# Optimization experiments

Hardware: AMD Instinct MI355X
Metric: run time of the kernel (lower is better)

The kernel has to match this reference:

```python
import jax, jax.numpy as jnp
import numpy as np

TEMP = 0.1
QUEUE_SIZE = 512
CUTOFF_KM = 25.0
EARTH_R_KM = 6371.0088


def _normalize(x, eps=1e-12):
    # F.normalize: x / max(||x||, eps)
    n = jnp.linalg.norm(x, axis=-1, keepdims=True)
    return x / jnp.maximum(n, eps)


def _haversine_km(g1, g2):
    # g1: (B,2) [lat,lon] degrees; g2: (S,2) -> (B,S) great-circle km
    r = jnp.pi / 180.0
    lat1 = g1[:, 0:1] * r
    lon1 = g1[:, 1:2] * r
    lat2 = g2[None, :, 0] * r
    lon2 = g2[None, :, 1] * r
    dlat = lat2 - lat1
    dlon = lon2 - lon1
    a = jnp.sin(dlat / 2) ** 2 + jnp.cos(lat1) * jnp.cos(lat2) * jnp.sin(dlon / 2) ** 2
    return 2.0 * EARTH_R_KM * jnp.arcsin(jnp.sqrt(jnp.clip(a, 0.0, 1.0)))


def setup_inputs() -> dict:
    key = jax.random.key(0)
    k = jax.random.split(key, 7)
    n_aug, B, D, S = 4, 256, 768, 65536
    V = jax.random.normal(k[0], (n_aug, B, D), jnp.float32)
    L = jax.random.normal(k[1], (B, D), jnp.float32)
    gps = jnp.concatenate([
        jax.random.uniform(k[2], (B, 1), jnp.float32, -90.0, 90.0),
        jax.random.uniform(k[3], (B, 1), jnp.float32, -180.0, 180.0)], axis=1)
    support_features = jax.random.normal(k[4], (S, D), jnp.float32)
    support_gps = jnp.concatenate([
        jax.random.uniform(k[5], (S, 1), jnp.float32, -90.0, 90.0),
        jax.random.uniform(k[6], (S, 1), jnp.float32, -180.0, 180.0)], axis=1)
    return {"V": V, "L": L, "gps": gps,
            "support_features": support_features, "support_gps": support_gps}


def reference(V, L, gps, support_features, support_gps):
    # org joint embedding always from V[0]; nearest neighbour over raw support feats
    org = _normalize(V[0] * L)                                   # (B,D)
    sim = org @ support_features.T                               # (B,S)
    nn_idx = jnp.argmax(sim, axis=1)                             # (B,)
    nn = _normalize(support_features[nn_idx])                    # (B,D)

    # augmented joints for j = 1..n_aug-1
    augs = _normalize(V[1:] * L[None])                           # (J,B,D)
    # numerator always uses V[1] (as in the original code), constant over j
    num = jnp.einsum('bd,bd->b', nn, augs[0]) / TEMP             # (B,)

    # in-batch denominator: sum_i exp(nn_b . aug_{j,i} / T)
    batch_den = jnp.exp(jnp.einsum('bd,jid->jbi', nn, augs) / TEMP).sum(axis=2)  # (J,B)

    # GPS-filtered negative queue: first QUEUE_SIZE support entries > 25 km away,
    # zero-padded (zero rows contribute exp(0) = 1, matching the torch code)
    mask = _haversine_km(gps, support_gps) > CUTOFF_KM           # (B,S)
    order = jnp.argsort(jnp.where(mask, 0, 1), axis=1)[:, :QUEUE_SIZE]  # stable: kept in original order
    valid = jnp.take_along_axis(mask, order, axis=1)             # (B,Q)
    qfeat = support_features[order] * valid[..., None]           # (B,Q,D)
    queue_den = jnp.exp(jnp.einsum('bd,bqd->bq', nn, qfeat) / TEMP).sum(axis=1)  # (B,)

    den = jnp.log(batch_den + queue_den[None, :])                # (J,B)
    loss = -(num[None, :] - den).sum() / V.shape[1]
    return loss
```

## Files before the change

kernel.cpp:

```cpp
#include <hip/hip_runtime.h>
#include <hip/hip_bf16.h>

#define B_ROWS 256
#define S_SUP  65536
#define D_DIM  768
#define QSZ    512
#define NCH    3
#define CHUNK_K 256
#define ACH_BYTES 131072

typedef short bf16x8 __attribute__((ext_vector_type(8)));
typedef float f32x4  __attribute__((ext_vector_type(4)));
typedef float f32x16 __attribute__((ext_vector_type(16)));

__device__ __forceinline__ bf16x8 cvt8(float4 a, float4 b) {
  bf16x8 r;
  r[0] = (short)(__float_as_uint(a.x) >> 16);
  r[1] = (short)(__float_as_uint(a.y) >> 16);
  r[2] = (short)(__float_as_uint(a.z) >> 16);
  r[3] = (short)(__float_as_uint(a.w) >> 16);
  r[4] = (short)(__float_as_uint(b.x) >> 16);
  r[5] = (short)(__float_as_uint(b.y) >> 16);
  r[6] = (short)(__float_as_uint(b.z) >> 16);
  r[7] = (short)(__float_as_uint(b.w) >> 16);
  return r;
}

__device__ __forceinline__ void gl_lds16(const void* g, void* l) {
  __builtin_amdgcn_global_load_lds(
      (const __attribute__((address_space(1))) unsigned int*)g,
      (__attribute__((address_space(3))) unsigned int*)l, 16, 0, 0);
}

__device__ __forceinline__ float block_sum(float v) {
  __shared__ float tmp[4];
  #pragma unroll
  for (int m = 32; m >= 1; m >>= 1) v += __shfl_xor(v, m, 64);
  __syncthreads();
  if ((threadIdx.x & 63) == 0) tmp[threadIdx.x >> 6] = v;
  __syncthreads();
  return tmp[0] + tmp[1] + tmp[2] + tmp[3];
}

__device__ __forceinline__ double block_sum_d(double v) {
  __shared__ double tmp[4];
  #pragma unroll
  for (int m = 32; m >= 1; m >>= 1) v += __shfl_xor(v, m, 64);
  __syncthreads();
  if ((threadIdx.x & 63) == 0) tmp[threadIdx.x >> 6] = v;
  __syncthreads();
  return tmp[0] + tmp[1] + tmp[2] + tmp[3];
}

__global__ __launch_bounds__(256) void init_kernel(unsigned long long* gmax, double* bden) {
  int t = threadIdx.x;
  gmax[t] = 0ull;
  for (int i = t; i < 3 * B_ROWS; i += 256) bden[i] = 0.0;
}

__global__ __launch_bounds__(256) void prep_kernel(const float* __restrict__ V,
                                                   const float* __restrict__ L,
                                                   unsigned short* __restrict__ orgb,
                                                   float* __restrict__ augs) {
  int jb = blockIdx.x;
  int j = jb >> 8, b = jb & 255;
  int tid = threadIdx.x;
  __shared__ float srow[D_DIM];
  const float* v = V + ((size_t)j * B_ROWS + b) * D_DIM;
  const float* l = L + (size_t)b * D_DIM;
  float p[3]; float ssq = 0.f;
  #pragma unroll
  for (int i = 0; i < 3; ++i) {
    int k = tid + 256 * i;
    p[i] = v[k] * l[k];
    ssq += p[i] * p[i];
  }
  ssq = block_sum(ssq);
  float inv = 1.0f / fmaxf(sqrtf(ssq), 1e-12f);
  if (j == 0) {
    #pragma unroll
    for (int i = 0; i < 3; ++i) srow[tid + 256 * i] = p[i] * inv;
    __syncthreads();
    if (tid < 96) {
      int k0 = tid * 8;
      float4 f0 = *(const float4*)&srow[k0];
      float4 f1 = *(const float4*)&srow[k0 + 4];
      bf16x8 hv = cvt8(f0, f1);
      int c = k0 >> 8, g = (k0 >> 3) & 31;
      *(bf16x8*)(orgb + c * 65536 + g * 2048 + b * 8) = hv;
    }
  } else {
    float* dst = augs + ((size_t)(j - 1) * B_ROWS + b) * D_DIM;
    #pragma unroll
    for (int i = 0; i < 3; ++i) dst[tid + 256 * i] = p[i] * inv;
  }
}

__global__ __launch_bounds__(512, 2) void sim_argmax_kernel(const unsigned short* __restrict__ orgb,
                                                            const float* __restrict__ sf,
                                                            unsigned long long* __restrict__ gmax) {
  const int tid = threadIdx.x;
  const int w   = tid >> 6;
  const int l   = tid & 63;
  const int h   = l >> 5;
  const int c31 = l & 31;
  const int s0  = blockIdx.x * 256;
  const int myrow = s0 + w * 32 + c31;

  __shared__ __align__(16) char smem[ACH_BYTES];

  f32x16 accs[8];
  #pragma unroll
  for (int t = 0; t < 8; ++t)
    #pragma unroll
    for (int r = 0; r < 16; ++r) accs[t][r] = 0.f;

  const char* sfb = (const char*)sf + (size_t)myrow * 3072 + h * 32;
  const char* agbase = (const char*)orgb + tid * 16;
  char* adst = smem + tid * 16;

  for (int c = 0; c < NCH; ++c) {
    {
      const char* g = agbase + c * ACH_BYTES;
      #pragma unroll
      for (int i = 0; i < 16; ++i)
        gl_lds16(g + i * 8192, adst + i * 8192);
    }
    __syncthreads();

    const char* brow = sfb + c * 1024;
    float4 nb0 = *(const float4*)(brow);
    float4 nb1 = *(const float4*)(brow + 16);
    #pragma unroll
    for (int ks = 0; ks < 16; ++ks) {
      float4 cb0 = nb0, cb1 = nb1;
      if (ks < 15) {
        nb0 = *(const float4*)(brow + (ks + 1) * 64);
        nb1 = *(const float4*)(brow + (ks + 1) * 64 + 16);
      }
      bf16x8 bf = cvt8(cb0, cb1);
      const char* ab = smem + (ks * 2 + h) * 4096 + c31 * 16;
      #pragma unroll
      for (int rt = 0; rt < 8; ++rt) {
        bf16x8 af = *(const bf16x8*)(ab + rt * 512);
        accs[rt] = __builtin_amdgcn_mfma_f32_32x32x16_bf16(af, bf, accs[rt], 0, 0, 0);
      }
    }
    __syncthreads();
  }

  float* smax = (float*)smem;
  int*   sidx = (int*)(smem + 8192);
  #pragma unroll
  for (int rt = 0; rt < 8; ++rt) {
    #pragma unroll
    for (int rg = 0; rg < 16; ++rg) {
      float v = accs[rt][rg];
      int idx = myrow;
      #pragma unroll
      for (int m = 1; m < 32; m <<= 1) {
        float ov = __shfl_xor(v, m, 64);
        int   oi = __shfl_xor(idx, m, 64);
        if (ov > v || (ov == v && oi < idx)) { v = ov; idx = oi; }
      }
      if (c31 == 0) {
        int row = rt * 32 + (rg & 3) + 8 * (rg >> 2) + 4 * h;
        smax[w * 256 + row] = v;
        sidx[w * 256 + row] = idx;
      }
    }
  }
  __syncthreads();
  if (tid < 256) {
    int row = tid;
    float v = smax[row]; int idx = sidx[row];
    #pragma unroll
    for (int w2 = 1; w2 < 8; ++w2) {
      float ov = smax[w2 * 256 + row]; int oi = sidx[w2 * 256 + row];
      if (ov > v || (ov == v && oi < idx)) { v = ov; idx = oi; }
    }
    unsigned u = __float_as_uint(v);
    unsigned key = (u & 0x80000000u) ? ~u : (u | 0x80000000u);
    unsigned long long packed = ((unsigned long long)key << 32) |
                                (unsigned long long)(0xFFFFFFFFu - (unsigned)idx);
    if (packed > gmax[row]) atomicMax(gmax + row, packed);
  }
}

__global__ __launch_bounds__(256) void nn_kernel(const unsigned long long* __restrict__ gmax,
                                                 const float* __restrict__ sf,
                                                 const float* __restrict__ augs,
                                                 float* __restrict__ nn,
                                                 float* __restrict__ nnT,
                                                 float* __restrict__ num) {
  int b = blockIdx.x, tid = threadIdx.x;
  int idx = (int)(0xFFFFFFFFu - (unsigned)(gmax[b] & 0xFFFFFFFFull));
  const float* row = sf + (size_t)idx * D_DIM;
  float p[3]; float ssq = 0.f;
  #pragma unroll
  for (int i = 0; i < 3; ++i) { p[i] = row[tid + 256 * i]; ssq += p[i] * p[i]; }
  ssq = block_sum(ssq);
  float inv = 1.0f / fmaxf(sqrtf(ssq), 1e-12f);
  const float* a0 = augs + (size_t)b * D_DIM;
  float dot = 0.f;
  #pragma unroll
  for (int i = 0; i < 3; ++i) {
    int k = tid + 256 * i;
    float nv = p[i] * inv;
    nn[(size_t)b * D_DIM + k] = nv;
    nnT[(size_t)k * B_ROWS + b] = nv;
    dot += nv * a0[k];
  }
  dot = block_sum(dot);
  if (tid == 0) num[b] = dot * 10.0f;
}

__global__ __launch_bounds__(256) void bden_kernel(const float* __restrict__ augs,
                                                   const float* __restrict__ nnT,
                                                   double* __restrict__ bden) {
  int jc = blockIdx.x;
  int j = jc >> 6, c = jc & 63;
  int i0 = c * 4;
  __shared__ float s_aug[4 * D_DIM];
  const float* src = augs + ((size_t)j * B_ROWS + i0) * D_DIM;
  for (int idx = threadIdx.x; idx < 4 * D_DIM; idx += 256) s_aug[idx] = src[idx];
  __syncthreads();
  int b = threadIdx.x;
  float a0 = 0.f, a1 = 0.f, a2 = 0.f, a3 = 0.f;
  for (int k = 0; k < D_DIM; ++k) {
    float nv = nnT[(size_t)k * B_ROWS + b];
    a0 += nv * s_aug[k];
    a1 += nv * s_aug[D_DIM + k];
    a2 += nv * s_aug[2 * D_DIM + k];
    a3 += nv * s_aug[3 * D_DIM + k];
  }
  double v = exp((double)a0 * 10.0) + exp((double)a1 * 10.0) +
             exp((double)a2 * 10.0) + exp((double)a3 * 10.0);
  atomicAdd(&bden[j * B_ROWS + b], v);
}

__global__ __launch_bounds__(256) void queue_kernel(const float* __restrict__ gps,
                                                    const float* __restrict__ sgps,
                                                    const float* __restrict__ sf,
                                                    const float* __restrict__ nn,
                                                    double* __restrict__ qden) {
  int b = blockIdx.x, tid = threadIdx.x;
  int w = tid >> 6, lane = tid & 63;
  __shared__ int qidx[QSZ];
  __shared__ int s_count;
  __shared__ int s_wcnt[4];
  __shared__ __align__(16) float s_nn[D_DIM];
  __shared__ double s_gsum[16];
  for (int k = tid; k < D_DIM; k += 256) s_nn[k] = nn[(size_t)b * D_DIM + k];
  if (tid == 0) s_count = 0;
  __syncthreads();

  const float r = 0.017453292519943295f;
  float lat1 = gps[b * 2 + 0] * r, lon1 = gps[b * 2 + 1] * r;
  float cl1 = cosf(lat1);
  int base = 0;
  while (true) {
    int count = s_count;
    if (count >= QSZ || base >= S_SUP) break;
    int s = base + tid;
    float lat2 = sgps[s * 2 + 0] * r, lon2 = sgps[s * 2 + 1] * r;
    float sdlat = sinf((lat2 - lat1) * 0.5f);
    float sdlon = sinf((lon2 - lon1) * 0.5f);
    float a = sdlat * sdlat + cl1 * cosf(lat2) * sdlon * sdlon;
    a = fminf(fmaxf(a, 0.f), 1.f);
    float d = 2.0f * 6371.0088f * asinf(sqrtf(a));
    bool valid = d > 25.0f;

    unsigned long long m = __ballot(valid);
    int wcnt = __popcll(m);
    if (lane == 0) s_wcnt[w] = wcnt;
    __syncthreads();
    int wbase = count;
    for (int i = 0; i < w; ++i) wbase += s_wcnt[i];
    int pos = wbase + __popcll(m & ((1ull << lane) - 1ull));
    if (valid && pos < QSZ) qidx[pos] = s;
    __syncthreads();
    if (tid == 0) {
      int total = s_wcnt[0] + s_wcnt[1] + s_wcnt[2] + s_wcnt[3];
      s_count = min(QSZ, count + total);
    }
    base += 256;
    __syncthreads();
  }
  int count = s_count;

  int g  = lane >> 4;
  int l2 = lane & 15;
  double acc = 0.0;
  const float4* nn4 = (const float4*)s_nn;
  for (int q = w * 4 + g; q < count; q += 16) {
    const float4* row = (const float4*)(sf + (size_t)qidx[q] * D_DIM);
    float dot = 0.f;
    #pragma unroll
    for (int i = 0; i < 12; ++i) {
      float4 a = row[l2 + 16 * i];
      float4 nv = nn4[l2 + 16 * i];
      dot += a.x * nv.x + a.y * nv.y + a.z * nv.z + a.w * nv.w;
    }
    #pragma unroll
    for (int m2 = 8; m2 >= 1; m2 >>= 1) dot += __shfl_xor(dot, m2, 16);
    if (l2 == 0) acc += exp((double)dot * 10.0);
  }
  if (l2 == 0) s_gsum[w * 4 + g] = acc;
  __syncthreads();
  if (tid == 0) {
    double t = (double)(QSZ - count);
    #pragma unroll
    for (int i = 0; i < 16; ++i) t += s_gsum[i];
    qden[b] = t;
  }
}

__global__ __launch_bounds__(256) void loss_kernel(const float* __restrict__ num,
                                                   const double* __restrict__ bden,
                                                   const double* __restrict__ qden,
                                                   float* __restrict__ out) {
  int b = threadIdx.x;
  double q = qden[b];
  double n = (double)num[b];
  double t = 0.0;
  #pragma unroll
  for (int j = 0; j < 3; ++j) t += n - log(bden[j * B_ROWS + b] + q);
  t = block_sum_d(t);
  if (b == 0) out[0] = (float)(-t / 256.0);
}

extern "C" void kernel_launch(void* const* d_in, const int* in_sizes, int n_in,
                              void* d_out, int out_size, void* d_ws, size_t ws_size,
                              hipStream_t stream) {
  const float* V    = (const float*)d_in[0];
  const float* L    = (const float*)d_in[1];
  const float* gps  = (const float*)d_in[2];
  const float* sf   = (const float*)d_in[3];
  const float* sgps = (const float*)d_in[4];
  float* out = (float*)d_out;

  char* ws = (char*)d_ws;
  size_t off = 0;
  unsigned short* orgb = (unsigned short*)(ws + off); off += 393216;
  float* augs = (float*)(ws + off); off += 2359296;
  float* nn   = (float*)(ws + off); off += 786432;
  float* nnT  = (float*)(ws + off); off += 786432;
  float* num  = (float*)(ws + off); off += 1024;
  double* bden = (double*)(ws + off); off += 6144;
  double* qden = (double*)(ws + off); off += 2048;
  unsigned long long* gmax = (unsigned long long*)(ws + off); off += 2048;

  init_kernel<<<1, 256, 0, stream>>>(gmax, bden);
  prep_kernel<<<1024, 256, 0, stream>>>(V, L, orgb, augs);
  sim_argmax_kernel<<<S_SUP / 256, 512, 0, stream>>>(orgb, sf, gmax);
  nn_kernel<<<B_ROWS, 256, 0, stream>>>(gmax, sf, augs, nn, nnT, num);
  bden_kernel<<<192, 256, 0, stream>>>(augs, nnT, bden);
  queue_kernel<<<B_ROWS, 256, 0, stream>>>(gps, sgps, sf, nn, qden);
  loss_kernel<<<1, 256, 0, stream>>>(num, bden, qden, out);
}
```

Baseline: 440.8 us.

## Restructure sim-argmax GEMM into 2x4 warp tiling with double-buffered LDS B tiles

Reworks the similarity/argmax kernel. Each warp now computes a 128x64 sub-tile, so A and B fragments are both reused across MFMAs. Support-feature rows are staged through XOR-swizzled, double-buffered LDS after bf16 conversion, with global loads issued two steps ahead, instead of each lane loading its own B fragment from global memory. The A (org) layout and phase size change to match four K-phases of 192. The aim is to cut redundant global traffic and hide load latency behind MFMA, at the cost of extra LDS writes and barriers per K-step.

```diff
diff --git a/kernel.cpp b/kernel.cpp
--- a/kernel.cpp
+++ b/kernel.cpp
@@ -5,9 +5,13 @@
 #define S_SUP  65536
 #define D_DIM  768
 #define QSZ    512
-#define NCH    3
-#define CHUNK_K 256
-#define ACH_BYTES 131072
+#define NPH    4
+#define BKP    192
+#define NS     6
+#define SK     32
+#define APH    98304
+#define BUF0   98304
+#define BUF1   114688
 
 typedef short bf16x8 __attribute__((ext_vector_type(8)));
 typedef float f32x4  __attribute__((ext_vector_type(4)));
@@ -86,8 +90,7 @@
       float4 f0 = *(const float4*)&srow[k0];
       float4 f1 = *(const float4*)&srow[k0 + 4];
       bf16x8 hv = cvt8(f0, f1);
-      int c = k0 >> 8, g = (k0 >> 3) & 31;
-      *(bf16x8*)(orgb + c * 65536 + g * 2048 + b * 8) = hv;
+      *(bf16x8*)(orgb + tid * 2048 + b * 8) = hv;
     }
   } else {
     float* dst = augs + ((size_t)(j - 1) * B_ROWS + b) * D_DIM;
@@ -104,59 +107,114 @@
   const int l   = tid & 63;
   const int h   = l >> 5;
   const int c31 = l & 31;
+  const int wr  = w & 1;
+  const int wc  = w >> 1;
   const int s0  = blockIdx.x * 256;
-  const int myrow = s0 + w * 32 + c31;
-
-  __shared__ __align__(16) char smem[ACH_BYTES];
-
-  f32x16 accs[8];
+
+  __shared__ __align__(16) char smem[131072];
+
+  f32x16 acc[8];
   #pragma unroll
   for (int t = 0; t < 8; ++t)
     #pragma unroll
-    for (int r = 0; r < 16; ++r) accs[t][r] = 0.f;
-
-  const char* sfb = (const char*)sf + (size_t)myrow * 3072 + h * 32;
-  const char* agbase = (const char*)orgb + tid * 16;
+    for (int r = 0; r < 16; ++r) acc[t][r] = 0.f;
+
+  const int bc_st = tid >> 1;
+  const int kh    = tid & 1;
+  const float* bsrc = sf + (size_t)(s0 + bc_st) * D_DIM + kh * 16;
+  const int pl0 = kh * 2, pl1 = kh * 2 + 1;
+  const int wslot0 = ((bc_st ^ pl0) & 255) * 16;
+  const int wslot1 = ((bc_st ^ pl1) & 255) * 16;
+
+  const char* agb = (const char*)orgb + tid * 16;
   char* adst = smem + tid * 16;
 
-  for (int c = 0; c < NCH; ++c) {
+  const int row_off = (wr * 128 + c31) * 16;
+  const int bc0 = wc * 64 + c31;
+  const int bc1 = bc0 + 32;
+
+  float4 p0, p1, p2, p3, q0, q1, q2, q3;
+
+#define LOADP(ph, s) do { const float4* gp = (const float4*)(bsrc + (ph) * BKP + (s) * SK); \
+    p0 = gp[0]; p1 = gp[1]; p2 = gp[2]; p3 = gp[3]; } while (0)
+#define LOADQ(ph, s) do { const float4* gp = (const float4*)(bsrc + (ph) * BKP + (s) * SK); \
+    q0 = gp[0]; q1 = gp[1]; q2 = gp[2]; q3 = gp[3]; } while (0)
+#define WRITEP(buf) do { *(bf16x8*)((buf) + pl0 * 4096 + wslot0) = cvt8(p0, p1); \
+    *(bf16x8*)((buf) + pl1 * 4096 + wslot1) = cvt8(p2, p3); } while (0)
+#define WRITEQ(buf) do { *(bf16x8*)((buf) + pl0 * 4096 + wslot0) = cvt8(q0, q1); \
+    *(bf16x8*)((buf) + pl1 * 4096 + wslot1) = cvt8(q2, q3); } while (0)
+#define BAR() do { asm volatile("s_waitcnt lgkmcnt(0)" ::: "memory"); \
+    __builtin_amdgcn_s_barrier(); __builtin_amdgcn_sched_barrier(0); } while (0)
+#define COMPUTE(si, buf) do { \
+    _Pragma("unroll") \
+    for (int g01 = 0; g01 < 2; ++g01) { \
+      const char* ap = smem + ((si) * 4 + g01 * 2 + h) * 4096 + row_off; \
+      bf16x8 a0 = *(const bf16x8*)(ap); \
+      bf16x8 a1 = *(const bf16x8*)(ap + 512); \
+      bf16x8 a2 = *(const bf16x8*)(ap + 1024); \
+      bf16x8 a3 = *(const bf16x8*)(ap + 1536); \
+      const int bpl = g01 * 2 + h; \
+      bf16x8 b0 = *(const bf16x8*)((buf) + bpl * 4096 + ((bc0 ^ bpl) & 255) * 16); \
+      bf16x8 b1 = *(const bf16x8*)((buf) + bpl * 4096 + ((bc1 ^ bpl) & 255) * 16); \
+      acc[0] = __builtin_amdgcn_mfma_f32_32x32x16_bf16(a0, b0, acc[0], 0, 0, 0); \
+      acc[1] = __builtin_amdgcn_mfma_f32_32x32x16_bf16(a0, b1, acc[1], 0, 0, 0); \
+      acc[2] = __builtin_amdgcn_mfma_f32_32x32x16_bf16(a1, b0, acc[2], 0, 0, 0); \
+      acc[3] = __builtin_amdgcn_mfma_f32_32x32x16_bf16(a1, b1, acc[3], 0, 0, 0); \
+      acc[4] = __builtin_amdgcn_mfma_f32_32x32x16_bf16(a2, b0, acc[4], 0, 0, 0); \
+      acc[5] = __builtin_amdgcn_mfma_f32_32x32x16_bf16(a2, b1, acc[5], 0, 0, 0); \
+      acc[6] = __builtin_amdgcn_mfma_f32_32x32x16_bf16(a3, b0, acc[6], 0, 0, 0); \
+      acc[7] = __builtin_amdgcn_mfma_f32_32x32x16_bf16(a3, b1, acc[7], 0, 0, 0); \
+    } } while (0)
+
+  char* const b0p = smem + BUF0;
+  char* const b1p = smem + BUF1;
+
+  for (int ph = 0; ph < NPH; ++ph) {
     {
-      const char* g = agbase + c * ACH_BYTES;
+      const char* g = agb + ph * APH;
       #pragma unroll
-      for (int i = 0; i < 16; ++i)
-        gl_lds16(g + i * 8192, adst + i * 8192);
-    }
-    __syncthreads();
-
-    const char* brow = sfb + c * 1024;
-    float4 nb0 = *(const float4*)(brow);
-    float4 nb1 = *(const float4*)(brow + 16);
-    #pragma unroll
-    for (int ks = 0; ks < 16; ++ks) {
-      float4 cb0 = nb0, cb1 = nb1;
-      if (ks < 15) {
-        nb0 = *(const float4*)(brow + (ks + 1) * 64);
-        nb1 = *(const float4*)(brow + (ks + 1) * 64 + 16);
+      for (int i = 0; i < 12; ++i) gl_lds16(g + i * 8192, adst + i * 8192);
+    }
+    LOADP(ph, 0);
+    LOADQ(ph, 1);
+    asm volatile("s_waitcnt vmcnt(8)" ::: "memory");
+    __builtin_amdgcn_s_barrier();
+    __builtin_amdgcn_sched_barrier(0);
+    WRITEP(b0p);
+    BAR();
+
+    #pragma unroll
+    for (int si = 0; si < NS; ++si) {
+      char* bufc = (si & 1) ? b1p : b0p;
+      char* bufn = (si & 1) ? b0p : b1p;
+      COMPUTE(si, bufc);
+      if (si < NS - 1) {
+        if (si & 1) WRITEP(bufn); else WRITEQ(bufn);
+        if (si + 2 < NS) { if (si & 1) LOADQ(ph, si + 2); else LOADP(ph, si + 2); }
       }
-      bf16x8 bf = cvt8(cb0, cb1);
-      const char* ab = smem + (ks * 2 + h) * 4096 + c31 * 16;
-      #pragma unroll
-      for (int rt = 0; rt < 8; ++rt) {
-        bf16x8 af = *(const bf16x8*)(ab + rt * 512);
-        accs[rt] = __builtin_amdgcn_mfma_f32_32x32x16_bf16(af, bf, accs[rt], 0, 0, 0);
-      }
-    }
-    __syncthreads();
-  }
+      BAR();
+    }
+  }
+
+#undef LOADP
+#undef LOADQ
+#undef WRITEP
+#undef WRITEQ
+#undef BAR
+#undef COMPUTE
 
   float* smax = (float*)smem;
-  int*   sidx = (int*)(smem + 8192);
-  #pragma unroll
-  for (int rt = 0; rt < 8; ++rt) {
+  int*   sidx = (int*)(smem + 4096);
+  #pragma unroll
+  for (int rt = 0; rt < 4; ++rt) {
     #pragma unroll
     for (int rg = 0; rg < 16; ++rg) {
-      float v = accs[rt][rg];
-      int idx = myrow;
+      float v0 = acc[rt * 2 + 0][rg];
+      float v1 = acc[rt * 2 + 1][rg];
+      int i0 = s0 + bc0;
+      int i1 = s0 + bc1;
+      float v; int idx;
+      if (v1 > v0) { v = v1; idx = i1; } else { v = v0; idx = i0; }
       #pragma unroll
       for (int m = 1; m < 32; m <<= 1) {
         float ov = __shfl_xor(v, m, 64);
@@ -164,26 +222,26 @@
         if (ov > v || (ov == v && oi < idx)) { v = ov; idx = oi; }
       }
       if (c31 == 0) {
-        int row = rt * 32 + (rg & 3) + 8 * (rg >> 2) + 4 * h;
-        smax[w * 256 + row] = v;
-        sidx[w * 256 + row] = idx;
+        int row = wr * 128 + rt * 32 + (rg & 3) + 8 * (rg >> 2) + 4 * h;
+        smax[wc * 256 + row] = v;
+        sidx[wc * 256 + row] = idx;
       }
     }
   }
   __syncthreads();
   if (tid < 256) {
-    int row = tid;
-    float v = smax[row]; int idx = sidx[row];
-    #pragma unroll
-    for (int w2 = 1; w2 < 8; ++w2) {
-      float ov = smax[w2 * 256 + row]; int oi = sidx[w2 * 256 + row];
+    int b = tid;
+    float v  = smax[b];  int idx = sidx[b];
+    #pragma unroll
+    for (int w2 = 1; w2 < 4; ++w2) {
+      float ov = smax[w2 * 256 + b]; int oi = sidx[w2 * 256 + b];
       if (ov > v || (ov == v && oi < idx)) { v = ov; idx = oi; }
     }
     unsigned u = __float_as_uint(v);
     unsigned key = (u & 0x80000000u) ? ~u : (u | 0x80000000u);
     unsigned long long packed = ((unsigned long long)key << 32) |
                                 (unsigned long long)(0xFFFFFFFFu - (unsigned)idx);
-    if (packed > gmax[row]) atomicMax(gmax + row, packed);
+    if (packed > gmax[b]) atomicMax(gmax + b, packed);
   }
 }
 
```

New measurement: 407.2 us. 1.08x faster.
